# Kernel tuning notes

Hardware: AMD Instinct MI355X
Metric: run time of the kernel (lower is better)

The kernel has to match this reference:

```python
import jax, jax.numpy as jnp
import numpy as np

NUM_ITER = 2
MIN_FILTER_REG = 1e-5
NUM_BINS = 10
BIN_DISP = 0.5
BG_MASK_VAL = 0.0
STEPLEN_REG = 0.0


def apply_filter(feat, filt):
    # feat: [1, S, C, H, W], filt: [S, NF, C, fh, fw] -> scores [1, S, NF, H, W]
    _, S, C, H, W = feat.shape
    NF, fh, fw = filt.shape[1], filt.shape[3], filt.shape[4]
    out = jax.lax.conv_general_dilated(
        feat.reshape(1, S * C, H, W),
        filt.reshape(S * NF, C, fh, fw),
        window_strides=(1, 1),
        padding=[(fh // 2, fh // 2), (fw // 2, fw // 2)],
        feature_group_count=S)
    return out.reshape(1, S, NF, H, W)


def apply_feat_transpose(feat, residuals, filt_shape):
    # gradient of apply_filter w.r.t. the filter (conv transpose on weights)
    zero = jnp.zeros(filt_shape, feat.dtype)
    _, vjp = jax.vjp(lambda w: apply_filter(feat, w), zero)
    return vjp(residuals)[0]


def distance_map(dH, dW, cy, cx):
    # pytracking DistanceMap: soft bin assignment of radial distance, [NUM_BINS, dH, dW]
    d0 = jnp.arange(dH, dtype=jnp.float32) - cy
    d1 = jnp.arange(dW, dtype=jnp.float32) - cx
    dist = jnp.sqrt(d0[:, None] ** 2 + d1[None, :] ** 2)
    bin_diff = dist[None] / BIN_DISP - jnp.arange(NUM_BINS, dtype=jnp.float32)[:, None, None]
    main = jax.nn.relu(1.0 - jnp.abs(bin_diff[:-1]))
    last = jnp.clip(1.0 + bin_diff[-1:], 0.0, 1.0)
    return jnp.concatenate([main, last], axis=0)


def unfold_map(full_map, H, W):
    # equivalent of F.unfold(...).view(H,W,H,W).flip((2,3)).permute(2,3,0,1)
    # map[i*W+j, y, x] = full_map[H-1-i+y, W-1-j+x]
    yy = (H - 1) - jnp.arange(H)[:, None] + jnp.arange(H)[None, :]  # [i, y]
    xx = (W - 1) - jnp.arange(W)[:, None] + jnp.arange(W)[None, :]  # [j, x]
    m = full_map[yy[:, None, :, None], xx[None, :, None, :]]        # [i, j, y, x]
    return m.reshape(1, 1, H * W, H, W)


def setup_inputs() -> dict:
    key = jax.random.key(0)
    k1, k2 = jax.random.split(key)
    S, C, H, W, fsz = 8, 256, 23, 23, 3
    NF = H * W
    filt = jax.random.normal(k1, (S, NF, C, fsz, fsz), jnp.float32) * 0.01
    feat = jax.random.normal(k2, (1, S, C, H, W), jnp.float32)
    # label_map_predictor init: gauss(sigma=1.0) over bin centers, min-subtracted
    d = jnp.arange(NUM_BINS, dtype=jnp.float32) * BIN_DISP
    g = jnp.exp(-0.5 * (d / 1.0) ** 2)
    w_label = g - g.min()
    w_spatial = jnp.ones((NUM_BINS,), jnp.float32)
    log_step_length = jnp.zeros((), jnp.float32)       # log(1.0)
    filter_reg = jnp.asarray(0.01, jnp.float32)
    return {"filter": filt, "feat": feat, "w_label": w_label, "w_spatial": w_spatial,
            "log_step_length": log_step_length, "filter_reg": filter_reg}


def reference(filter, feat, w_label, w_spatial, log_step_length, filter_reg):
    f = filter
    _, S, C, H, W = feat.shape
    NF = f.shape[1]
    dH, dW = 2 * H - 1, 2 * W - 1
    bins = distance_map(dH, dW, dH // 2, dW // 2)                 # [B, dH, dW]
    label_full = jnp.einsum('b,bhw->hw', w_label, bins)           # 1x1 conv
    spatial_full = jnp.einsum('b,bhw->hw', w_spatial, bins)
    label_map = unfold_map(label_full, H, W)                      # [1,1,NF,H,W]
    spatial_weight = unfold_map(spatial_full, H, W)
    tm = (1.0 - BG_MASK_VAL) * jnp.eye(NF, dtype=f.dtype).reshape(1, 1, NF, H, W) + BG_MASK_VAL
    step_length = jnp.exp(log_step_length)
    reg_weight = jnp.maximum(filter_reg * filter_reg, MIN_FILTER_REG ** 2)

    for _ in range(NUM_ITER):
        scores = apply_filter(feat, f)                            # [1,S,NF,H,W]
        # LeakyReluPar activation parameterized by target mask
        scores_act = (1.0 - tm) * 0.5 * jnp.abs(scores) + (1.0 + tm) * 0.5 * scores
        score_mask = (1.0 - tm) * 0.5 * jnp.sign(jax.lax.stop_gradient(scores)) + (1.0 + tm) * 0.5
        loss_residuals = spatial_weight * (scores_act - label_map)
        mapped_residuals = score_mask * (spatial_weight * loss_residuals)
        filter_grad = apply_feat_transpose(feat, mapped_residuals, f.shape) + reg_weight * f
        scores_grad = apply_filter(feat, filter_grad)
        scores_grad = spatial_weight * (score_mask * scores_grad)
        alpha_num = (filter_grad * filter_grad).reshape(S, NF, -1).sum(-1)   # [S, NF]
        alpha_den = jnp.maximum(
            (scores_grad * scores_grad).reshape(S, NF, -1).sum(-1) + reg_weight * alpha_num, 1e-8)
        alpha_den = alpha_den + STEPLEN_REG * alpha_num
        alpha = alpha_num / alpha_den
        f = f - step_length * alpha.reshape(S, NF, 1, 1, 1) * filter_grad
    return f
```

## Files before the change

### kernel.cpp

```cpp
#include <hip/hip_runtime.h>
#include <math.h>

#define NF   529
#define K9   2304
#define NP   544
#define DMAP 45

typedef unsigned short ush;
typedef unsigned int u32;
typedef __bf16 bf8_t __attribute__((ext_vector_type(8)));
typedef float f4_t __attribute__((ext_vector_type(4)));
typedef ush ush8 __attribute__((ext_vector_type(8)));


__device__ __forceinline__ ush f2bf(float f) {
  union { float f; u32 u; } v; v.f = f;
  u32 r = v.u + 0x7fffu + ((v.u >> 16) & 1u);
  return (ush)(r >> 16);
}
__device__ __forceinline__ float bf2f(ush h) {
  union { u32 u; float f; } v; v.u = ((u32)h) << 16;
  return v.f;
}
__device__ __forceinline__ void async16(const void* g, void* l) {
  __builtin_amdgcn_global_load_lds((const __attribute__((address_space(1))) u32*)g,
                                   (__attribute__((address_space(3))) u32*)l, 16, 0, 0);
}

__global__ void build_maps(const float* __restrict__ wl, const float* __restrict__ wsp,
                           float* __restrict__ labelF, float* __restrict__ spatialF) {
  int idx = blockIdx.x * blockDim.x + threadIdx.x;
  if (idx >= DMAP * DMAP) return;
  int h = idx / DMAP, w = idx % DMAP;
  float dy = (float)(h - 22), dx = (float)(w - 22);
  float dist = sqrtf(dy * dy + dx * dx);
  float lab = 0.f, sp = 0.f;
#pragma unroll
  for (int b = 0; b < 9; ++b) {
    float bd = dist * 2.f - (float)b;
    float wt = fmaxf(0.f, 1.f - fabsf(bd));
    lab += wl[b] * wt;
    sp  += wsp[b] * wt;
  }
  float bd = dist * 2.f - 9.f;
  float wt = fminf(fmaxf(1.f + bd, 0.f), 1.f);
  lab += wl[9] * wt;
  sp  += wsp[9] * wt;
  labelF[idx] = lab;
  spatialF[idx] = sp;
}

__global__ void convert_f(const float* __restrict__ filt, float* __restrict__ F,
                          ush* __restrict__ Fhl) {
  int g = blockIdx.x * 256 + threadIdx.x;
  int row = g / 288;
  int kk = (g - row * 288) * 8;
  int s = row / NF, m = row - s * NF;
  const float4* fp = (const float4*)(filt + (size_t)row * K9 + kk);
  float4 a = fp[0], b = fp[1];
  float4* Fp = (float4*)(F + (size_t)row * K9 + kk);
  Fp[0] = a; Fp[1] = b;
  float vv[8] = {a.x, a.y, a.z, a.w, b.x, b.y, b.z, b.w};
  ush8 h, lo;
#pragma unroll
  for (int i = 0; i < 8; ++i) {
    ush hh = f2bf(vv[i]);
    h[i] = hh;
    lo[i] = f2bf(vv[i] - bf2f(hh));
  }
  size_t o = ((size_t)s * 576 + m) * (2 * K9) + (kk >> 5) * 64 + (kk & 31);
  *(ush8*)(Fhl + o) = h;
  *(ush8*)(Fhl + o + 32) = lo;
}

__global__ void im2col_pack(const float* __restrict__ feat,
                            ush* __restrict__ Xbhl, ush* __restrict__ XThl) {
  __shared__ float T[64][65];
  int s = blockIdx.z, k0 = blockIdx.y * 64, yx0 = blockIdx.x * 64;
  int t = threadIdx.x;
  int r = t >> 2, c4 = (t & 3) * 16;
  int k = k0 + r;
  int ck = k / 9, j = k - ck * 9;
  int dy = j / 3 - 1, dx = j - (j / 3) * 3 - 1;
  const float* fb = feat + ((size_t)s * 256 + ck) * 529;
  float v[16];
#pragma unroll
  for (int i = 0; i < 16; ++i) {
    int yx = yx0 + c4 + i;
    float vv = 0.f;
    if (yx < NF) {
      int yy = yx / 23;
      int y = yy + dy, x = yx - yy * 23 + dx;
      if (y >= 0 && y < 23 && x >= 0 && x < 23) vv = fb[y * 23 + x];
    }
    v[i] = vv;
    T[r][c4 + i] = vv;
  }
  int c0 = yx0 + c4;
  if (c0 < NP) {
    size_t o = ((size_t)s * K9 + k) * (2 * NP) + (c0 >> 5) * 64 + (c0 & 31);
    ush8 h[2], lo[2];
#pragma unroll
    for (int gg = 0; gg < 2; ++gg)
#pragma unroll
      for (int i = 0; i < 8; ++i) {
        float vv = v[gg * 8 + i];
        ush hh = f2bf(vv);
        h[gg][i] = hh;
        lo[gg][i] = f2bf(vv - bf2f(hh));
      }
    *(ush8*)(Xbhl + o) = h[0];
    *(ush8*)(Xbhl + o + 8) = h[1];
    *(ush8*)(Xbhl + o + 32) = lo[0];
    *(ush8*)(Xbhl + o + 40) = lo[1];
  }
  __syncthreads();
  int kc = k0 + c4;
  size_t o2 = ((size_t)s * 640 + yx0 + r) * (2 * K9) + (kc >> 5) * 64 + (kc & 31);
  ush8 h2[2], l2[2];
#pragma unroll
  for (int gg = 0; gg < 2; ++gg)
#pragma unroll
    for (int i = 0; i < 8; ++i) {
      float vv = T[c4 + gg * 8 + i][r];
      ush hh = f2bf(vv);
      h2[gg][i] = hh;
      l2[gg][i] = f2bf(vv - bf2f(hh));
    }
  *(ush8*)(XThl + o2) = h2[0];
  *(ush8*)(XThl + o2 + 8) = h2[1];
  *(ush8*)(XThl + o2 + 32) = l2[0];
  *(ush8*)(XThl + o2 + 40) = l2[1];
}

template <int KTOT, int ASPL, int BSPL, int MODE, int SKC, int CH, int BPG, int GX>
__launch_bounds__(256, 4)
__global__ void gemm128(const ush* __restrict__ Ahl, const ush* __restrict__ Bhl,
                        float* __restrict__ Cp,
                        const float* __restrict__ F, const float* __restrict__ frp,
                        ush* __restrict__ FGhl, float* __restrict__ numb,
                        const int arows) {
  __shared__ ush As[ASPL][128 * 32];
  __shared__ ush Bs[BSPL][128 * 32];

  const int tid = threadIdx.x;
  const int w = tid >> 6, l = tid & 63;
  const int wm = w & 1, wn = w >> 1;
  const int q = l >> 4, c = l & 15;

  const int xcd = blockIdx.x & 7;
  const int t = blockIdx.x >> 3;
  const int g = xcd + 8 * (t / BPG);
  const int j = t % BPG;
  const int s = g / SKC, sk = g % SKC;
  const int x = j % GX, y = j / GX;
  const int m0 = x * 128, n0 = y * 128;

  const ush* A0 = Ahl + (size_t)s * arows * (2 * KTOT);
  const ush* B0 = Bhl + (size_t)s * ((MODE == 2) ? K9 : 640) * (2 * KTOT);

  const int srow = w * 16 + (l >> 2);
  const int scol = (l & 3) * 8;
  const int ssw  = ((((l & 3) - (l >> 3)) & 3)) * 8;

  f4_t acc[4][4];
#pragma unroll
  for (int i = 0; i < 4; ++i)
#pragma unroll
    for (int jj = 0; jj < 4; ++jj) acc[i][jj] = (f4_t){0.f, 0.f, 0.f, 0.f};

  for (int ch = 0; ch < CH; ++ch) {
    const int k2 = (sk * CH + ch) * 64;
#pragma unroll
    for (int i = 0; i < 2; ++i) {
      size_t ro = (size_t)(m0 + i * 64 + srow) * (2 * KTOT) + k2 + ssw;
      async16(A0 + ro, &As[0][(i * 64 + srow) * 32 + scol]);
      if (ASPL == 2) async16(A0 + ro + 32, &As[1][(i * 64 + srow) * 32 + scol]);
    }
#pragma unroll
    for (int i = 0; i < 2; ++i) {
      size_t ro = (size_t)(n0 + i * 64 + srow) * (2 * KTOT) + k2 + ssw;
      async16(B0 + ro, &Bs[0][(i * 64 + srow) * 32 + scol]);
      if (BSPL == 2) async16(B0 + ro + 32, &Bs[1][(i * 64 + srow) * 32 + scol]);
    }
    __syncthreads();

    const int slotA = (((q + (c >> 1)) & 3)) * 8;
    bf8_t av[ASPL][4], bv[BSPL][4];
#pragma unroll
    for (int pp = 0; pp < ASPL; ++pp)
#pragma unroll
      for (int ti = 0; ti < 4; ++ti)
        av[pp][ti] = *(const bf8_t*)&As[pp][(wm * 64 + ti * 16 + c) * 32 + slotA];
#pragma unroll
    for (int pp = 0; pp < BSPL; ++pp)
#pragma unroll
      for (int tj = 0; tj < 4; ++tj)
        bv[pp][tj] = *(const bf8_t*)&Bs[pp][(wn * 64 + tj * 16 + c) * 32 + slotA];

#pragma unroll
    for (int ti = 0; ti < 4; ++ti)
#pragma unroll
      for (int tj = 0; tj < 4; ++tj) {
        acc[ti][tj] = __builtin_amdgcn_mfma_f32_16x16x32_bf16(av[0][ti], bv[0][tj], acc[ti][tj], 0, 0, 0);
        if (ASPL == 2)
          acc[ti][tj] = __builtin_amdgcn_mfma_f32_16x16x32_bf16(av[1][ti], bv[0][tj], acc[ti][tj], 0, 0, 0);
        if (BSPL == 2)
          acc[ti][tj] = __builtin_amdgcn_mfma_f32_16x16x32_bf16(av[0][ti], bv[1][tj], acc[ti][tj], 0, 0, 0);
      }
    __syncthreads();
  }

  if (MODE == 0) {
    float* C = Cp + (size_t)(sk * 8 + s) * 640 * 640;
#pragma unroll
    for (int ti = 0; ti < 4; ++ti)
#pragma unroll
      for (int tj = 0; tj < 4; ++tj)
#pragma unroll
        for (int r = 0; r < 4; ++r) {
          int m = m0 + wm * 64 + ti * 16 + q * 4 + r;
          int n = n0 + wn * 64 + tj * 16 + c;
          __builtin_nontemporal_store(acc[ti][tj][r], &C[(size_t)m * 640 + n]);
        }
  } else {
    float reg = fmaxf(frp[0] * frp[0], 1e-10f);
#pragma unroll
    for (int ti = 0; ti < 4; ++ti) {
      float ps[4] = {0.f, 0.f, 0.f, 0.f};
      int mb = m0 + wm * 64 + ti * 16 + q * 4;
#pragma unroll
      for (int tj = 0; tj < 4; ++tj) {
        int n = n0 + wn * 64 + tj * 16 + c;
#pragma unroll
        for (int r = 0; r < 4; ++r) {
          int m = mb + r;
          if (m < NF) {
            float v = acc[ti][tj][r] + reg * F[((size_t)s * NF + m) * K9 + n];
            size_t o = ((size_t)s * 576 + m) * (2 * K9) + ((n >> 5) * 64) + (n & 31);
            ush h = f2bf(v);
            FGhl[o] = h;
            FGhl[o + 32] = f2bf(v - bf2f(h));
            ps[r] += v * v;
          }
        }
      }
#pragma unroll
      for (int r = 0; r < 4; ++r) {
        float pp = ps[r];
        pp += __shfl_xor(pp, 1); pp += __shfl_xor(pp, 2);
        pp += __shfl_xor(pp, 4); pp += __shfl_xor(pp, 8);
        if (c == 0 && (mb + r) < NF) atomicAdd(&numb[s * NF + mb + r], pp);
      }
    }
  }
}

__global__ void reduce_epi1(const float* __restrict__ Cp,
                            const float* __restrict__ labelF, const float* __restrict__ spatialF,
                            ush* __restrict__ Rbhl, ush* __restrict__ Mb) {
  int row = blockIdx.x;
  int s = row / NF, m = row - s * NF;
  int a = m / 23, b = m - a * 23;
  const size_t sp = (size_t)8 * 640 * 640;
  const float* C = Cp + ((size_t)s * 640 + m) * 640;
  for (int n = threadIdx.x; n < NF; n += 256) {
    float v = __builtin_nontemporal_load(&C[n]) +
              __builtin_nontemporal_load(&C[sp + n]) +
              __builtin_nontemporal_load(&C[2 * sp + n]) +
              __builtin_nontemporal_load(&C[3 * sp + n]);
    int yy = n / 23, xx = n - yy * 23;
    int idx = (22 + yy - a) * DMAP + (22 + xx - b);
    float sw = spatialF[idx], lm = labelF[idx];
    float sa, msk;
    if (m == n) { sa = v; msk = 1.f; }
    else {
      sa = 0.5f * fabsf(v) + 0.5f * v;
      msk = (v > 0.f) ? 1.f : ((v < 0.f) ? 0.f : 0.5f);
    }
    float rv = msk * sw * sw * (sa - lm);
    size_t o = ((size_t)s * 640 + m) * (2 * NP) + ((n >> 5) * 64) + (n & 31);
    ush h = f2bf(rv);
    Rbhl[o] = h;
    Rbhl[o + 32] = f2bf(rv - bf2f(h));
    Mb[((size_t)s * NF + m) * NP + n] = f2bf(msk);
  }
}

__global__ void reduce_epi3(const float* __restrict__ Cp,
                            const float* __restrict__ spatialF, const ush* __restrict__ Mb,
                            float* __restrict__ denb) {
  int row = blockIdx.x;
  int s = row / NF, m = row - s * NF;
  int a = m / 23, b = m - a * 23;
  const size_t sp = (size_t)8 * 640 * 640;
  const float* C = Cp + ((size_t)s * 640 + m) * 640;
  float ss = 0.f;
  for (int n = threadIdx.x; n < NF; n += 256) {
    float v = __builtin_nontemporal_load(&C[n]) +
              __builtin_nontemporal_load(&C[sp + n]) +
              __builtin_nontemporal_load(&C[2 * sp + n]) +
              __builtin_nontemporal_load(&C[3 * sp + n]);
    int yy = n / 23, xx = n - yy * 23;
    int idx = (22 + yy - a) * DMAP + (22 + xx - b);
    float sw = spatialF[idx];
    float msk = bf2f(Mb[((size_t)s * NF + m) * NP + n]);
    float z = sw * msk * v;
    ss += z * z;
  }
  __shared__ float red[256];
  red[threadIdx.x] = ss; __syncthreads();
  for (int st = 128; st > 0; st >>= 1) {
    if (threadIdx.x < st) red[threadIdx.x] += red[threadIdx.x + st];
    __syncthreads();
  }
  if (threadIdx.x == 0) denb[row] = red[0];
}

__global__ void update_f(float* __restrict__ F, const ush* __restrict__ FGhl,
                         const float* __restrict__ numb, const float* __restrict__ denb,
                         const float* __restrict__ lsp, const float* __restrict__ frp,
                         ush* __restrict__ Fhl) {
  int g = blockIdx.x * 256 + threadIdx.x;
  int row = g / 288;
  int kk = (g - row * 288) * 8;
  int s = row / NF, m = row - s * NF;
  float reg = fmaxf(frp[0] * frp[0], 1e-10f);
  float nm = numb[row], dn = denb[row];
  float alpha = nm / fmaxf(dn + reg * nm, 1e-8f);
  float sa = expf(lsp[0]) * alpha;
  size_t o = ((size_t)s * 576 + m) * (2 * K9) + (kk >> 5) * 64 + (kk & 31);
  ush8 gh = *(const ush8*)(FGhl + o);
  ush8 gl = *(const ush8*)(FGhl + o + 32);
  float4* Fp = (float4*)(F + (size_t)row * K9 + kk);
  float4 a = Fp[0], b = Fp[1];
  float f[8] = {a.x, a.y, a.z, a.w, b.x, b.y, b.z, b.w};
  ush8 h, lo;
#pragma unroll
  for (int i = 0; i < 8; ++i) {
    f[i] -= sa * (bf2f(gh[i]) + bf2f(gl[i]));
    ush hh = f2bf(f[i]);
    h[i] = hh;
    lo[i] = f2bf(f[i] - bf2f(hh));
  }
  Fp[0] = (float4){f[0], f[1], f[2], f[3]};
  Fp[1] = (float4){f[4], f[5], f[6], f[7]};
  *(ush8*)(Fhl + o) = h;
  *(ush8*)(Fhl + o + 32) = lo;
}

extern "C" void kernel_launch(void* const* d_in, const int* in_sizes, int n_in,
                              void* d_out, int out_size, void* d_ws, size_t ws_size,
                              hipStream_t stream) {
  const float* filt = (const float*)d_in[0];
  const float* feat = (const float*)d_in[1];
  const float* wl   = (const float*)d_in[2];
  const float* wsp  = (const float*)d_in[3];
  const float* lsp  = (const float*)d_in[4];
  const float* frp  = (const float*)d_in[5];
  float* F = (float*)d_out;

  float* fb       = (float*)d_ws;
  float* labelF   = fb;
  float* spatialF = fb + 2048;
  float* numden   = fb + 4096;
  ush* cur = (ush*)(fb + 4096 + 4 * 4240);

  const size_t szF  = (size_t)8 * 576 * (2 * K9);
  const size_t szXT = (size_t)8 * 640 * (2 * K9);
  const size_t szXb = (size_t)8 * K9 * (2 * NP);
  const size_t szRb = (size_t)8 * 640 * (2 * NP);
  const size_t szMb = (size_t)8 * NF * NP;

  ush* Fhl  = cur;           cur += szF;
  ush* FGhl = cur;           cur += szF;
  ush* XThl = cur;           cur += szXT;
  ush* Xbhl = cur;           cur += szXb;
  ush* Rbhl = cur;           cur += szRb;
  ush* Mb   = cur;           cur += szMb;
  float* Cp = (float*)((((size_t)cur) + 15) & ~(size_t)15);

  build_maps<<<8, 256, 0, stream>>>(wl, wsp, labelF, spatialF);
  hipMemsetAsync(numden, 0, 4 * 4240 * sizeof(float), stream);
  convert_f<<<4761, 256, 0, stream>>>(filt, F, Fhl);
  im2col_pack<<<dim3(10, 36, 8), 256, 0, stream>>>(feat, Xbhl, XThl);

  for (int it = 0; it < 2; ++it) {
    float* numb = numden + it * 2 * 4240;
    float* denb = numb + 4240;
    gemm128<K9, 2, 2, 0, 4, 18, 25, 5><<<800, 256, 0, stream>>>(
        Fhl, XThl, Cp, nullptr, nullptr, nullptr, nullptr, 576);
    reduce_epi1<<<8 * NF, 256, 0, stream>>>(Cp, labelF, spatialF, Rbhl, Mb);
    gemm128<NP, 2, 2, 2, 1, 17, 90, 5><<<720, 256, 0, stream>>>(
        Rbhl, Xbhl, nullptr, F, frp, FGhl, numb, 640);
    gemm128<K9, 1, 1, 0, 4, 18, 25, 5><<<800, 256, 0, stream>>>(
        FGhl, XThl, Cp, nullptr, nullptr, nullptr, nullptr, 576);
    reduce_epi3<<<8 * NF, 256, 0, stream>>>(Cp, spatialF, Mb, denb);
    update_f<<<4761, 256, 0, stream>>>(F, FGhl, numb, denb, lsp, frp, Fhl);
  }
}
```

Measured before the change: 506.0 us.

## Load GEMM operands directly from global into registers, dropping LDS staging

```diff
diff --git a/kernel.cpp b/kernel.cpp
--- a/kernel.cpp
+++ b/kernel.cpp
@@ -21,10 +21,6 @@
 __device__ __forceinline__ float bf2f(ush h) {
   union { u32 u; float f; } v; v.u = ((u32)h) << 16;
   return v.f;
-}
-__device__ __forceinline__ void async16(const void* g, void* l) {
-  __builtin_amdgcn_global_load_lds((const __attribute__((address_space(1))) u32*)g,
-                                   (__attribute__((address_space(3))) u32*)l, 16, 0, 0);
 }
 
 __global__ void build_maps(const float* __restrict__ wl, const float* __restrict__ wsp,
@@ -134,15 +130,12 @@
 }
 
 template <int KTOT, int ASPL, int BSPL, int MODE, int SKC, int CH, int BPG, int GX>
-__launch_bounds__(256, 4)
+__launch_bounds__(256, (ASPL + BSPL >= 4) ? 3 : 4)
 __global__ void gemm128(const ush* __restrict__ Ahl, const ush* __restrict__ Bhl,
                         float* __restrict__ Cp,
                         const float* __restrict__ F, const float* __restrict__ frp,
                         ush* __restrict__ FGhl, float* __restrict__ numb,
                         const int arows) {
-  __shared__ ush As[ASPL][128 * 32];
-  __shared__ ush Bs[BSPL][128 * 32];
-
   const int tid = threadIdx.x;
   const int w = tid >> 6, l = tid & 63;
   const int wm = w & 1, wn = w >> 1;
@@ -159,9 +152,8 @@
   const ush* A0 = Ahl + (size_t)s * arows * (2 * KTOT);
   const ush* B0 = Bhl + (size_t)s * ((MODE == 2) ? K9 : 640) * (2 * KTOT);
 
-  const int srow = w * 16 + (l >> 2);
-  const int scol = (l & 3) * 8;
-  const int ssw  = ((((l & 3) - (l >> 3)) & 3)) * 8;
+  const ush* Ar = A0 + (size_t)(m0 + wm * 64 + c) * (2 * KTOT) + q * 8;
+  const ush* Br = B0 + (size_t)(n0 + wn * 64 + c) * (2 * KTOT) + q * 8;
 
   f4_t acc[4][4];
 #pragma unroll
@@ -171,32 +163,20 @@
 
   for (int ch = 0; ch < CH; ++ch) {
     const int k2 = (sk * CH + ch) * 64;
-#pragma unroll
-    for (int i = 0; i < 2; ++i) {
-      size_t ro = (size_t)(m0 + i * 64 + srow) * (2 * KTOT) + k2 + ssw;
-      async16(A0 + ro, &As[0][(i * 64 + srow) * 32 + scol]);
-      if (ASPL == 2) async16(A0 + ro + 32, &As[1][(i * 64 + srow) * 32 + scol]);
-    }
-#pragma unroll
-    for (int i = 0; i < 2; ++i) {
-      size_t ro = (size_t)(n0 + i * 64 + srow) * (2 * KTOT) + k2 + ssw;
-      async16(B0 + ro, &Bs[0][(i * 64 + srow) * 32 + scol]);
-      if (BSPL == 2) async16(B0 + ro + 32, &Bs[1][(i * 64 + srow) * 32 + scol]);
-    }
-    __syncthreads();
-
-    const int slotA = (((q + (c >> 1)) & 3)) * 8;
+
     bf8_t av[ASPL][4], bv[BSPL][4];
 #pragma unroll
-    for (int pp = 0; pp < ASPL; ++pp)
-#pragma unroll
-      for (int ti = 0; ti < 4; ++ti)
-        av[pp][ti] = *(const bf8_t*)&As[pp][(wm * 64 + ti * 16 + c) * 32 + slotA];
-#pragma unroll
-    for (int pp = 0; pp < BSPL; ++pp)
-#pragma unroll
-      for (int tj = 0; tj < 4; ++tj)
-        bv[pp][tj] = *(const bf8_t*)&Bs[pp][(wn * 64 + tj * 16 + c) * 32 + slotA];
+    for (int ti = 0; ti < 4; ++ti) {
+      const ush* p = Ar + (size_t)(ti * 16) * (2 * KTOT) + k2;
+      av[0][ti] = *(const bf8_t*)p;
+      if (ASPL == 2) av[1][ti] = *(const bf8_t*)(p + 32);
+    }
+#pragma unroll
+    for (int tj = 0; tj < 4; ++tj) {
+      const ush* p = Br + (size_t)(tj * 16) * (2 * KTOT) + k2;
+      bv[0][tj] = *(const bf8_t*)p;
+      if (BSPL == 2) bv[1][tj] = *(const bf8_t*)(p + 32);
+    }
 
 #pragma unroll
     for (int ti = 0; ti < 4; ++ti)
@@ -208,7 +188,6 @@
         if (BSPL == 2)
           acc[ti][tj] = __builtin_amdgcn_mfma_f32_16x16x32_bf16(av[0][ti], bv[1][tj], acc[ti][tj], 0, 0, 0);
       }
-    __syncthreads();
   }
 
   if (MODE == 0) {
```

New measurement: 866.1 us. +71.1%, slower.
